# Optimization experiments

Hardware: AMD Instinct MI355X
Metric: run time of the kernel (lower is better)

Reference implementation:

```python
import jax, jax.numpy as jnp
import numpy as np

N, E, C, H = 50000, 250000, 7, 64
D = C + 2  # node feature dim after concatenating labels


def _mlp2(x, w1, b1, w2, b2):
    return jnp.maximum(x @ w1 + b1, 0.0) @ w2 + b2


def _lin(key, fi, fo, bias=True):
    lim = 1.0 / np.sqrt(fi)
    kw, kb = jax.random.split(key)
    w = jax.random.uniform(kw, (fi, fo), jnp.float32, -lim, lim)
    if bias:
        b = jax.random.uniform(kb, (fo,), jnp.float32, -lim, lim)
        return w, b
    return w


def setup_inputs() -> dict:
    key = jax.random.key(0)
    ks = jax.random.split(key, 16)
    v = jax.random.normal(ks[0], (N, C), jnp.float32)
    labels = jnp.zeros((N, 2), jnp.float32).at[0, 1].set(1.0)  # node 0 is the goal
    edge_index = jax.random.randint(ks[1], (2, E), 0, N)
    hx_w1, hx_b1 = _lin(ks[2], 4 * D, H)
    hx_w2, hx_b2 = _lin(ks[3], H, H)
    hy_w1, hy_b1 = _lin(ks[4], 3 * D, H)
    hy_w2, hy_b2 = _lin(ks[5], H, H)
    fx_w1, fx_b1 = _lin(ks[6], 4 * H, H)
    fx_w2, fx_b2 = _lin(ks[7], H, H)
    fy_w1, fy_b1 = _lin(ks[8], 3 * H, H)
    fy_w2, fy_b2 = _lin(ks[9], H, H)
    feta_w1, feta_b1 = _lin(ks[10], H, H)
    feta_w2, feta_b2 = _lin(ks[11], H, H)
    feta_w3 = _lin(ks[12], H, 1, bias=False)
    return dict(v=v, labels=labels, edge_index=edge_index, loop=3,
                hx_w1=hx_w1, hx_b1=hx_b1, hx_w2=hx_w2, hx_b2=hx_b2,
                hy_w1=hy_w1, hy_b1=hy_b1, hy_w2=hy_w2, hy_b2=hy_b2,
                fx_w1=fx_w1, fx_b1=fx_b1, fx_w2=fx_w2, fx_b2=fx_b2,
                fy_w1=fy_w1, fy_b1=fy_b1, fy_w2=fy_w2, fy_b2=fy_b2,
                feta_w1=feta_w1, feta_b1=feta_b1, feta_w2=feta_w2, feta_b2=feta_b2,
                feta_w3=feta_w3)


def reference(v, labels, edge_index, loop,
              hx_w1, hx_b1, hx_w2, hx_b2,
              hy_w1, hy_b1, hy_w2, hy_b2,
              fx_w1, fx_b1, fx_w2, fx_b2,
              fy_w1, fy_b1, fy_w2, fy_b2,
              feta_w1, feta_b1, feta_w2, feta_b2, feta_w3):
    n = v.shape[0]
    vc = jnp.concatenate([v, labels], axis=-1)              # [N, D]
    goal = vc[jnp.argmax(labels[:, 1])][None, :]             # [1, D]
    d = vc - goal
    x = _mlp2(jnp.concatenate([vc, jnp.broadcast_to(goal, vc.shape), d, d * d], -1),
              hx_w1, hx_b1, hx_w2, hx_b2)                    # [N, H]
    src, dst = edge_index[0], edge_index[1]
    vi, vj = vc[src], vc[dst]
    y = _mlp2(jnp.concatenate([vj - vi, vj, vi], -1), hy_w1, hy_b1, hy_w2, hy_b2)  # [E, H]
    for _ in range(loop):
        # MPNN (PyG default flow): x_j = source = edge_index[0], x_i = target = edge_index[1]
        xj_m, xi_m = x[src], x[dst]
        m = _mlp2(jnp.concatenate([xj_m - xi_m, xj_m, xi_m, y], -1),
                  fx_w1, fx_b1, fx_w2, fx_b2)                # [E, H]
        agg = jax.ops.segment_max(m, dst, num_segments=n)    # scatter-max to targets; empty -> -inf
        x = jnp.maximum(x, agg)                              # -inf absorbed by max with x
        xi, xj = x[src], x[dst]                              # Explorer: i=edge_index[0], j=edge_index[1]
        y = jnp.maximum(y, _mlp2(jnp.concatenate([xj - xi, xj, xi], -1),
                                 fy_w1, fy_b1, fy_w2, fy_b2))
    h = jnp.maximum(x @ feta_w1 + feta_b1, 0.0)
    h = jnp.maximum(h @ feta_w2 + feta_b2, 0.0)
    return h @ feta_w3                                       # [N, 1]
```

## Files before the change

### kernel.cpp

```cpp
#include <hip/hip_runtime.h>
#include <math.h>

typedef unsigned short u16;
typedef unsigned int u32;
typedef unsigned long long u64;
typedef __attribute__((ext_vector_type(8))) _Float16 f16x8;
typedef __attribute__((ext_vector_type(2))) _Float16 f16x2;
typedef __attribute__((ext_vector_type(4))) float f32x4;

union U8h { f16x8 v; f16x2 p[4]; u32 u[4]; _Float16 s[8]; };
union U4h { _Float16 s[4]; u64 u; };

__device__ __forceinline__ void atomicMaxF(float* addr, float val) {
  if (val >= 0.0f) {
    atomicMax((int*)addr, __float_as_int(val));
  } else {
    atomicMin((unsigned int*)addr, (unsigned int)__float_as_int(val));
  }
}

__device__ __forceinline__ f16x2 pk(float a, float b) {
  return __builtin_bit_cast(f16x2, __builtin_amdgcn_cvt_pkrtz(a, b));
}

__device__ __forceinline__ void dec8h(const float* f, U8h& h, U8h& l) {
#pragma unroll
// ... 113 lines not shown
  if (c < 64) {
    float s = hxb1[c];
#pragma unroll
    for (int k = 0; k < 9; ++k) s += g[k] * hxw1[(9 + k) * 64 + c];
    b1p[c] = s;
  }
}

__global__ __launch_bounds__(256) void k_prep(const float* __restrict__ fxw1, const float* __restrict__ fxw2,
                                              const float* __restrict__ fyw1, const float* __restrict__ fyw2,
                                              const float* __restrict__ hyw1, const float* __restrict__ hyw2,
                                              const float* __restrict__ hxw1, const float* __restrict__ hxw2,
                                              const float* __restrict__ few1, const float* __restrict__ few2,
                                              _Float16* __restrict__ wp, u64* __restrict__ goalkey) {
  if (blockIdx.x == 0 && threadIdx.x == 0) *goalkey = 0;
  _Float16* fxB1 = wp;
  _Float16* fxB2 = wp + 12288;
  _Float16* fyB1 = wp + 16384;
  _Float16* fyB2 = wp + 24576;
  _Float16* hyB1 = wp + 28672;
  _Float16* hyB2 = wp + 30720;
  _Float16* hxB1 = wp + 34816;
  _Float16* hxB2 = wp + 36864;
  _Float16* feB1 = wp + 40960;
  _Float16* feB2 = wp + 45056;
  int tid = blockIdx.x * 256 + threadIdx.x;
  int which, id;
  _Float16* oh;
  if (tid < 1536)      { which = 0; id = tid;        oh = fxB1; }
  else if (tid < 2048) { which = 1; id = tid - 1536; oh = fxB2; }
  else if (tid < 3072) { which = 2; id = tid - 2048; oh = fyB1; }
  else if (tid < 3584) { which = 3; id = tid - 3072; oh = fyB2; }
  else if (tid < 3840) { which = 4; id = tid - 3584; oh = hyB1; }
  else if (tid < 4352) { which = 5; id = tid - 3840; oh = hyB2; }
  else if (tid < 4608) { which = 6; id = tid - 4352; oh = hxB1; }
  else if (tid < 5120) { which = 7; id = tid - 4608; oh = hxB2; }
  else if (tid < 5632) { which = 8; id = tid - 5120; oh = feB1; }
  else if (tid < 6144) { which = 9; id = tid - 5632; oh = feB2; }
  else return;
  int lane = id & 63;
  int q = lane >> 4, col = lane & 15;
  int c = id >> 8, t = (id >> 6) & 3;
#pragma unroll
  for (int j = 0; j < 8; ++j) {
    int k = c * 32 + q * 8 + j;
    int n = t * 16 + col;
    float w;
    if (which == 0) {
      w = (k < 64)  ? fxw1[k * 64 + n] + fxw1[(k + 64) * 64 + n]
        : (k < 128) ? fxw1[(k + 64) * 64 + n] - fxw1[(k - 64) * 64 + n]
                    : fxw1[(k + 64) * 64 + n];
    } else if (which == 1) {
      w = fxw2[k * 64 + n];
// ... 2 lines not shown
                   : fyw1[(k + 64) * 64 + n] - fyw1[(k - 64) * 64 + n];
    } else if (which == 3) {
      w = fyw2[k * 64 + n];
    } else if (which == 4) {
      if (k <= 8)                  w = hyw1[k * 64 + n] + hyw1[(k + 9) * 64 + n];
      else if (k >= 16 && k <= 24) w = hyw1[(k + 2) * 64 + n] - hyw1[(k - 16) * 64 + n];
      else                         w = 0.f;
    } else if (which == 5) {
      w = hyw2[k * 64 + n];
    } else if (which == 6) {
      w = (k < 9) ? hxw1[k * 64 + n] : (k < 27) ? hxw1[(k + 9) * 64 + n] : 0.f;
    } else if (which == 7) {
      w = hxw2[k * 64 + n];
    } else if (which == 8) {
      w = few1[k * 64 + n];
    } else {
      w = few2[k * 64 + n];
    }
    oh[id * 8 + j] = (_Float16)w;
  }
}

__global__ __launch_bounds__(256) void k_scan1(const int* __restrict__ deg, int N,
                                               int* __restrict__ bsum) {
  __shared__ int red[256];
  int b = blockIdx.x;
  int s = 0;
  for (int i = threadIdx.x; i < 1024; i += 256) {
    int idx = b * 1024 + i;
    s += (idx < N) ? deg[idx] : 0;
  }
  red[threadIdx.x] = s; __syncthreads();
// ... 42 lines not shown
                                                 int* __restrict__ cursor,
                                                 int* __restrict__ srcp, int* __restrict__ dstp) {
  int e = blockIdx.x * 256 + threadIdx.x;
  if (e < E) {
    int d = dst[e];
    int pos = atomicAdd(&cursor[d], 1);
    srcp[pos] = src[e];
    dstp[pos] = d;
  }
}

__global__ __launch_bounds__(256) void k_hx2(
    const float* __restrict__ vcp, const float* __restrict__ goal,
    const _Float16* __restrict__ B1, const float* __restrict__ b1p,
    const _Float16* __restrict__ B2, const float* __restrict__ b2,
    float* __restrict__ xout, float* __restrict__ xout2, _Float16* __restrict__ xh, int N) {
  __shared__ float hbuf[4][16 * 68];
  const int lane = threadIdx.x & 63;
  const int wv = threadIdx.x >> 6;
  const int m = lane & 15, q = lane >> 4;
  const int base = blockIdx.x * 64 + wv * 16;
  int node = base + m; if (node >= N) node = N - 1;
  float vc[12];
  *(float4*)(vc + 0) = *(const float4*)(vcp + (size_t)node * 16);
  *(float4*)(vc + 4) = *(const float4*)(vcp + (size_t)node * 16 + 4);
  *(float4*)(vc + 8) = *(const float4*)(vcp + (size_t)node * 16 + 8);
  float gl[9];
#pragma unroll
  for (int i = 0; i < 9; ++i) gl[i] = goal[i];
  float f[8];
#pragma unroll
// ... 53 lines not shown
  int row = base + m;
  if (row < N) {
    float ov[16];
    const float* orow = hb + m * 68 + q * 16;
    *(float4*)(ov + 0)  = *(const float4*)(orow);
    *(float4*)(ov + 4)  = *(const float4*)(orow + 4);
    *(float4*)(ov + 8)  = *(const float4*)(orow + 8);
    *(float4*)(ov + 12) = *(const float4*)(orow + 12);
    float* p1 = xout + (size_t)row * 64 + q * 16;
    float* p2 = xout2 + (size_t)row * 64 + q * 16;
#pragma unroll
    for (int i = 0; i < 4; ++i) {
      *(float4*)(p1 + i * 4) = *(const float4*)(ov + i * 4);
      *(float4*)(p2 + i * 4) = *(const float4*)(ov + i * 4);
    }
    U8h X0, X1;
    conv8_rne(ov + 0, X0);
    conv8_rne(ov + 8, X1);
    *(f16x8*)(xh + (size_t)row * 64 + q * 16)     = X0.v;
    *(f16x8*)(xh + (size_t)row * 64 + q * 16 + 8) = X1.v;
  }
}

__global__ __launch_bounds__(256) void k_cc(const float4* __restrict__ s,
                                            float4* __restrict__ d,
                                            _Float16* __restrict__ h16, int n4) {
  int i = blockIdx.x * 256 + threadIdx.x;
  if (i < n4) {
    float4 v = s[i];
    d[i] = v;
    U4h o;
    o.s[0] = (_Float16)v.x; o.s[1] = (_Float16)v.y;
    o.s[2] = (_Float16)v.z; o.s[3] = (_Float16)v.w;
    *(u64*)(h16 + (size_t)i * 4) = o.u;
  }
}

__global__ __launch_bounds__(256) void k_hyfx(
    const float* __restrict__ vcp, const _Float16* __restrict__ xh,
    const int* __restrict__ src, const int* __restrict__ dst,
    const _Float16* __restrict__ hB1, const float* __restrict__ hb1,
    const _Float16* __restrict__ hB2, const float* __restrict__ hb2,
    const _Float16* __restrict__ xB1, const float* __restrict__ xb1,
    const _Float16* __restrict__ xB2, const float* __restrict__ xb2,
    _Float16* __restrict__ y, float* __restrict__ xnew, int E) {
  __shared__ float hbuf[4][16 * 68];
  const int lane = threadIdx.x & 63;
  const int wv = threadIdx.x >> 6;
  const int m = lane & 15, q = lane >> 4;
  const int base = blockIdx.x * 64 + wv * 16;
  int em = base + m; if (em >= E) em = E - 1;
  const int si = src[em], di = dst[em];
  const int row = base + m;
  const bool live = row < E;

  const int node = (q < 2) ? di : si;
  const float* p = vcp + (size_t)node * 16 + (q & 1) * 8;
  float f[8];
  *(float4*)(f + 0) = *(const float4*)(p);
  *(float4*)(f + 4) = *(const float4*)(p + 4);
  const _Float16* ps = xh + (size_t)si * 64 + q * 8;
  const _Float16* pd = xh + (size_t)di * 64 + q * 8;
  U8h Xs0, Xs1, Xd0, Xd1;
  Xs0.v = *(const f16x8*)ps;         Xs1.v = *(const f16x8*)(ps + 32);
  Xd0.v = *(const f16x8*)pd;         Xd1.v = *(const f16x8*)(pd + 32);

  U8h Ah, Al;
  dec8h(f, Ah, Al);

  f32x4 acc[4];
#pragma unroll
  for (int t = 0; t < 4; ++t) { float bv = hb1[t * 16 + m]; acc[t] = (f32x4){bv, bv, bv, bv}; }
#pragma unroll
  for (int t = 0; t < 4; ++t) {
    f16x8 b = *(const f16x8*)(hB1 + ((size_t)t * 64 + lane) * 8);
    acc[t] = __builtin_amdgcn_mfma_f32_16x16x32_f16(Ah.v, b, acc[t], 0, 0, 0);
    acc[t] = __builtin_amdgcn_mfma_f32_16x16x32_f16(Al.v, b, acc[t], 0, 0, 0);
  }

  float* hb = hbuf[wv];
#pragma unroll
  for (int t = 0; t < 4; ++t)
#pragma unroll
    for (int r = 0; r < 4; ++r)
      hb[(q * 4 + r) * 68 + t * 16 + m] = fmaxf(acc[t][r], 0.f);

  float fh[16];
  load_row(hb + m * 68 + q * 8, fh);
  U8h H0, H1;
  conv8_rne(fh + 0, H0);
  conv8_rne(fh + 8, H1);

  f32x4 o[4];
#pragma unroll
  for (int t = 0; t < 4; ++t) { float bv = hb2[t * 16 + m]; o[t] = (f32x4){bv, bv, bv, bv}; }
#pragma unroll
  for (int t = 0; t < 4; ++t) {
    f16x8 b0 = *(const f16x8*)(hB2 + ((size_t)(0 * 4 + t) * 64 + lane) * 8);
    f16x8 b1_ = *(const f16x8*)(hB2 + ((size_t)(1 * 4 + t) * 64 + lane) * 8);
    o[t] = __builtin_amdgcn_mfma_f32_16x16x32_f16(H0.v, b0, o[t], 0, 0, 0);
    o[t] = __builtin_amdgcn_mfma_f32_16x16x32_f16(H1.v, b1_, o[t], 0, 0, 0);
  }

#pragma unroll
  for (int t = 0; t < 4; ++t)
#pragma unroll
    for (int r = 0; r < 4; ++r)
      hb[(q * 4 + r) * 68 + t * 16 + m] = o[t][r];

  float nv[16];
  load_row(hb + m * 68 + q * 8, nv);
  U8h Yh0, Yh1;
  conv8_rne(nv + 0, Yh0);
  conv8_rne(nv + 8, Yh1);
  if (live) {
    size_t yo = (size_t)row * 64 + q * 8;
    *(f16x8*)(y + yo)      = Yh0.v;
    *(f16x8*)(y + yo + 32) = Yh1.v;
  }

  f32x4 acc2[4];
#pragma unroll
  for (int t = 0; t < 4; ++t) { float bv = xb1[t * 16 + m]; acc2[t] = (f32x4){bv, bv, bv, bv}; }
#pragma unroll
  for (int t = 0; t < 4; ++t) {
    f16x8 b0 = *(const f16x8*)(xB1 + ((size_t)(0 * 4 + t) * 64 + lane) * 8);
    f16x8 b1_ = *(const f16x8*)(xB1 + ((size_t)(1 * 4 + t) * 64 + lane) * 8);
    f16x8 b2_ = *(const f16x8*)(xB1 + ((size_t)(2 * 4 + t) * 64 + lane) * 8);
    f16x8 b3_ = *(const f16x8*)(xB1 + ((size_t)(3 * 4 + t) * 64 + lane) * 8);
    f16x8 b4_ = *(const f16x8*)(xB1 + ((size_t)(4 * 4 + t) * 64 + lane) * 8);
    f16x8 b5_ = *(const f16x8*)(xB1 + ((size_t)(5 * 4 + t) * 64 + lane) * 8);
    acc2[t] = __builtin_amdgcn_mfma_f32_16x16x32_f16(Xs0.v, b0, acc2[t], 0, 0, 0);
    acc2[t] = __builtin_amdgcn_mfma_f32_16x16x32_f16(Xs1.v, b1_, acc2[t], 0, 0, 0);
    acc2[t] = __builtin_amdgcn_mfma_f32_16x16x32_f16(Xd0.v, b2_, acc2[t], 0, 0, 0);
    acc2[t] = __builtin_amdgcn_mfma_f32_16x16x32_f16(Xd1.v, b3_, acc2[t], 0, 0, 0);
    acc2[t] = __builtin_amdgcn_mfma_f32_16x16x32_f16(Yh0.v, b4_, acc2[t], 0, 0, 0);
    acc2[t] = __builtin_amdgcn_mfma_f32_16x16x32_f16(Yh1.v, b5_, acc2[t], 0, 0, 0);
  }

#pragma unroll
  for (int t = 0; t < 4; ++t)
#pragma unroll
    for (int r = 0; r < 4; ++r)
      hb[(q * 4 + r) * 68 + t * 16 + m] = fmaxf(acc2[t][r], 0.f);

  float fh2[16];
  load_row(hb + m * 68 + q * 8, fh2);
  U8h G0, G1;
  conv8_rne(fh2 + 0, G0);
  conv8_rne(fh2 + 8, G1);

  f32x4 o2[4];
#pragma unroll
  for (int t = 0; t < 4; ++t) { float bv = xb2[t * 16 + m]; o2[t] = (f32x4){bv, bv, bv, bv}; }
#pragma unroll
  for (int t = 0; t < 4; ++t) {
    f16x8 b0 = *(const f16x8*)(xB2 + ((size_t)(0 * 4 + t) * 64 + lane) * 8);
    f16x8 b1_ = *(const f16x8*)(xB2 + ((size_t)(1 * 4 + t) * 64 + lane) * 8);
    o2[t] = __builtin_amdgcn_mfma_f32_16x16x32_f16(G0.v, b0, o2[t], 0, 0, 0);
    o2[t] = __builtin_amdgcn_mfma_f32_16x16x32_f16(G1.v, b1_, o2[t], 0, 0, 0);
  }

  int dd[4];
  int e0 = base + q * 4;
#pragma unroll
  for (int r = 0; r < 4; ++r) {
    int e2 = e0 + r;
    dd[r] = (e2 < E) ? dst[e2] : -1;
  }
  RunCtx rc = run_ctx(dd, lane, q);
#pragma unroll
  for (int t = 0; t < 4; ++t) emit_t(o2[t], dd, rc, lane, m, t, xnew);
}

__global__ __launch_bounds__(256) void k_fyfx(
    const _Float16* __restrict__ xh, _Float16* __restrict__ y,
    const int* __restrict__ src, const int* __restrict__ dst,
    const _Float16* __restrict__ yB1, const float* __restrict__ yb1,
    const _Float16* __restrict__ yB2, const float* __restrict__ yb2,
    const _Float16* __restrict__ xB1, const float* __restrict__ xb1,
    const _Float16* __restrict__ xB2, const float* __restrict__ xb2,
    float* __restrict__ xnew, int E, int storeY) {
  __shared__ float hbuf[4][16 * 68];
  const int lane = threadIdx.x & 63;
  const int wv = threadIdx.x >> 6;
  const int m = lane & 15, q = lane >> 4;
  const int base = blockIdx.x * 64 + wv * 16;
  int em = base + m; if (em >= E) em = E - 1;
  const int si = src[em], di = dst[em];
  const int row = base + m;
  const bool live = row < E;

  const _Float16* ps = xh + (size_t)si * 64 + q * 8;
  const _Float16* pd = xh + (size_t)di * 64 + q * 8;
  U8h Xs0, Xs1, Xd0, Xd1;
  Xs0.v = *(const f16x8*)ps;         Xs1.v = *(const f16x8*)(ps + 32);
  Xd0.v = *(const f16x8*)pd;         Xd1.v = *(const f16x8*)(pd + 32);
  U8h Ho0, Ho1;
  {
    size_t yo = (size_t)em * 64 + q * 8;
    Ho0.v = *(const f16x8*)(y + yo);  Ho1.v = *(const f16x8*)(y + yo + 32);
  }

  f32x4 acc[4];
#pragma unroll
  for (int t = 0; t < 4; ++t) { float bv = yb1[t * 16 + m]; acc[t] = (f32x4){bv, bv, bv, bv}; }
#pragma unroll
  for (int t = 0; t < 4; ++t) {
    f16x8 b0 = *(const f16x8*)(yB1 + ((size_t)(0 * 4 + t) * 64 + lane) * 8);
    f16x8 b1_ = *(const f16x8*)(yB1 + ((size_t)(1 * 4 + t) * 64 + lane) * 8);
    f16x8 b2_ = *(const f16x8*)(yB1 + ((size_t)(2 * 4 + t) * 64 + lane) * 8);
    f16x8 b3_ = *(const f16x8*)(yB1 + ((size_t)(3 * 4 + t) * 64 + lane) * 8);
    acc[t] = __builtin_amdgcn_mfma_f32_16x16x32_f16(Xd0.v, b0, acc[t], 0, 0, 0);
    acc[t] = __builtin_amdgcn_mfma_f32_16x16x32_f16(Xd1.v, b1_, acc[t], 0, 0, 0);
    acc[t] = __builtin_amdgcn_mfma_f32_16x16x32_f16(Xs0.v, b2_, acc[t], 0, 0, 0);
    acc[t] = __builtin_amdgcn_mfma_f32_16x16x32_f16(Xs1.v, b3_, acc[t], 0, 0, 0);
  }

  float* hb = hbuf[wv];
#pragma unroll
  for (int t = 0; t < 4; ++t)
#pragma unroll
    for (int r = 0; r < 4; ++r)
      hb[(q * 4 + r) * 68 + t * 16 + m] = fmaxf(acc[t][r], 0.f);

  float fh[16];
  load_row(hb + m * 68 + q * 8, fh);
  U8h H0, H1;
  conv8_rne(fh + 0, H0);
  conv8_rne(fh + 8, H1);

  f32x4 o[4];
#pragma unroll
  for (int t = 0; t < 4; ++t) { float bv = yb2[t * 16 + m]; o[t] = (f32x4){bv, bv, bv, bv}; }
#pragma unroll
  for (int t = 0; t < 4; ++t) {
    f16x8 b0 = *(const f16x8*)(yB2 + ((size_t)(0 * 4 + t) * 64 + lane) * 8);
    f16x8 b1_ = *(const f16x8*)(yB2 + ((size_t)(1 * 4 + t) * 64 + lane) * 8);
    o[t] = __builtin_amdgcn_mfma_f32_16x16x32_f16(H0.v, b0, o[t], 0, 0, 0);
    o[t] = __builtin_amdgcn_mfma_f32_16x16x32_f16(H1.v, b1_, o[t], 0, 0, 0);
  }

#pragma unroll
  for (int t = 0; t < 4; ++t)
#pragma unroll
    for (int r = 0; r < 4; ++r)
      hb[(q * 4 + r) * 68 + t * 16 + m] = o[t][r];

  float nv[16];
  load_row(hb + m * 68 + q * 8, nv);
#pragma unroll
  for (int i = 0; i < 8; ++i) {
    nv[i]     = fmaxf((float)Ho0.s[i], nv[i]);
    nv[8 + i] = fmaxf((float)Ho1.s[i], nv[8 + i]);
  }
  U8h Yh0, Yh1;
  conv8_rne(nv + 0, Yh0);
  conv8_rne(nv + 8, Yh1);
  if (live && storeY) {
    size_t yo = (size_t)row * 64 + q * 8;
    *(f16x8*)(y + yo)      = Yh0.v;
    *(f16x8*)(y + yo + 32) = Yh1.v;
  }

  f32x4 acc2[4];
#pragma unroll
  for (int t = 0; t < 4; ++t) { float bv = xb1[t * 16 + m]; acc2[t] = (f32x4){bv, bv, bv, bv}; }
#pragma unroll
  for (int t = 0; t < 4; ++t) {
    f16x8 b0 = *(const f16x8*)(xB1 + ((size_t)(0 * 4 + t) * 64 + lane) * 8);
    f16x8 b1_ = *(const f16x8*)(xB1 + ((size_t)(1 * 4 + t) * 64 + lane) * 8);
    f16x8 b2_ = *(const f16x8*)(xB1 + ((size_t)(2 * 4 + t) * 64 + lane) * 8);
    f16x8 b3_ = *(const f16x8*)(xB1 + ((size_t)(3 * 4 + t) * 64 + lane) * 8);
    f16x8 b4_ = *(const f16x8*)(xB1 + ((size_t)(4 * 4 + t) * 64 + lane) * 8);
    f16x8 b5_ = *(const f16x8*)(xB1 + ((size_t)(5 * 4 + t) * 64 + lane) * 8);
    acc2[t] = __builtin_amdgcn_mfma_f32_16x16x32_f16(Xs0.v, b0, acc2[t], 0, 0, 0);
    acc2[t] = __builtin_amdgcn_mfma_f32_16x16x32_f16(Xs1.v, b1_, acc2[t], 0, 0, 0);
    acc2[t] = __builtin_amdgcn_mfma_f32_16x16x32_f16(Xd0.v, b2_, acc2[t], 0, 0, 0);
    acc2[t] = __builtin_amdgcn_mfma_f32_16x16x32_f16(Xd1.v, b3_, acc2[t], 0, 0, 0);
    acc2[t] = __builtin_amdgcn_mfma_f32_16x16x32_f16(Yh0.v, b4_, acc2[t], 0, 0, 0);
    acc2[t] = __builtin_amdgcn_mfma_f32_16x16x32_f16(Yh1.v, b5_, acc2[t], 0, 0, 0);
  }

#pragma unroll
  for (int t = 0; t < 4; ++t)
#pragma unroll
    for (int r = 0; r < 4; ++r)
      hb[(q * 4 + r) * 68 + t * 16 + m] = fmaxf(acc2[t][r], 0.f);

  float fh2[16];
  load_row(hb + m * 68 + q * 8, fh2);
  U8h G0, G1;
  conv8_rne(fh2 + 0, G0);
  conv8_rne(fh2 + 8, G1);

  f32x4 o2[4];
#pragma unroll
  for (int t = 0; t < 4; ++t) { float bv = xb2[t * 16 + m]; o2[t] = (f32x4){bv, bv, bv, bv}; }
#pragma unroll
  for (int t = 0; t < 4; ++t) {
    f16x8 b0 = *(const f16x8*)(xB2 + ((size_t)(0 * 4 + t) * 64 + lane) * 8);
    f16x8 b1_ = *(const f16x8*)(xB2 + ((size_t)(1 * 4 + t) * 64 + lane) * 8);
    o2[t] = __builtin_amdgcn_mfma_f32_16x16x32_f16(G0.v, b0, o2[t], 0, 0, 0);
    o2[t] = __builtin_amdgcn_mfma_f32_16x16x32_f16(G1.v, b1_, o2[t], 0, 0, 0);
  }

  int dd[4];
  int e0 = base + q * 4;
#pragma unroll
  for (int r = 0; r < 4; ++r) {
    int e2 = e0 + r;
    dd[r] = (e2 < E) ? dst[e2] : -1;
  }
  RunCtx rc = run_ctx(dd, lane, q);
#pragma unroll
  for (int t = 0; t < 4; ++t) emit_t(o2[t], dd, rc, lane, m, t, xnew);
}

__global__ __launch_bounds__(256) void k_feta2(
// ... 96 lines not shown
  const float* feta_w2 = (const float*)d_in[22];
  const float* feta_b2 = (const float*)d_in[23];
  const float* feta_w3 = (const float*)d_in[24];

  int N = in_sizes[0] / 7;
  int E = in_sizes[2] / 2;
  const int* src = ei;
  const int* dst = ei + E;

  char* wsb = (char*)d_ws;
  float* goal = (float*)wsb;
  u64* goalkey = (u64*)(wsb + 64);
  float* b1p = (float*)(wsb + 96);
  float* xa = (float*)(wsb + 512);
  float* xb = xa + (size_t)N * 64;
  _Float16* xh = (_Float16*)(xb + (size_t)N * 64);
  _Float16* y = xh + (size_t)N * 64;
  _Float16* wp = y + (size_t)E * 64;
  float* vcp = (float*)(wp + 49152);
  int* deg = (int*)(vcp + (size_t)N * 16);
  int* cursor = deg + N;
  int* srcp = cursor + N;
  int* dstp = srcp + E;
  int* bsum = dstp + E;

  _Float16* fxB1 = wp;          _Float16* fxB2 = wp + 12288;
  _Float16* fyB1 = wp + 16384;  _Float16* fyB2 = wp + 24576;
  _Float16* hyB1 = wp + 28672;  _Float16* hyB2 = wp + 30720;
  _Float16* hxB1 = wp + 34816;  _Float16* hxB2 = wp + 36864;
  _Float16* feB1 = wp + 40960;  _Float16* feB2 = wp + 45056;

  int SB = (N + 1023) / 1024;

  hipMemsetAsync(deg, 0, (size_t)N * 4, stream);
  k_prep<<<24, 256, 0, stream>>>(fx_w1, fx_w2, fy_w1, fy_w2, hy_w1, hy_w2,
                                 hx_w1, hx_w2, feta_w1, feta_w2, wp, goalkey);
  k_vch<<<(N * 16 + 255) / 256, 256, 0, stream>>>(v, labels, vcp, N, dst, E, deg, goalkey);
  k_goal2b<<<1, 64, 0, stream>>>(v, labels, goalkey, hx_w1, hx_b1, goal, b1p);
  k_scan1<<<SB, 256, 0, stream>>>(deg, N, bsum);
  k_scan3<<<SB, 256, 0, stream>>>(deg, bsum, N, cursor);
  k_scatter<<<(E + 255) / 256, 256, 0, stream>>>(src, dst, E, cursor, srcp, dstp);

  k_hx2<<<(N + 63) / 64, 256, 0, stream>>>(vcp, goal, hxB1, b1p, hxB2, hx_b2, xa, xb, xh, N);

  int EB = (E + 63) / 64;
  k_hyfx<<<EB, 256, 0, stream>>>(vcp, xh, srcp, dstp,
                                 hyB1, hy_b1, hyB2, hy_b2,
                                 fxB1, fx_b1, fxB2, fx_b2, y, xb, E);
  k_cc<<<(N * 16 + 255) / 256, 256, 0, stream>>>((const float4*)xb, (float4*)xa, xh, N * 16);
  k_fyfx<<<EB, 256, 0, stream>>>(xh, y, srcp, dstp,
                                 fyB1, fy_b1, fyB2, fy_b2,
                                 fxB1, fx_b1, fxB2, fx_b2, xa, E, 1);
  k_cc<<<(N * 16 + 255) / 256, 256, 0, stream>>>((const float4*)xa, (float4*)xb, xh, N * 16);
  k_fyfx<<<EB, 256, 0, stream>>>(xh, y, srcp, dstp,
                                 fyB1, fy_b1, fyB2, fy_b2,
                                 fxB1, fx_b1, fxB2, fx_b2, xb, E, 0);

  k_feta2<<<(N + 63) / 64, 256, 0, stream>>>(xb, feB1, feta_b1, feB2, feta_b2, feta_w3,
                                             (float*)d_out, N);
}
```

Measured before the change: 342.4 us.

## Precompute per-node first-layer projections and gather them in edge kernels

The first-layer matmuls of the edge MLPs are linear in the source and destination node features, so they are split into per-node projections. A new node kernel computes these with MFMA and stores four 64-wide fp16 slots per node (256 halves). The edge kernel then gathers and adds the projected slots instead of running the K=128 or K=384 MFMAs per edge, keeping only the y-part of the fx first layer and the second layers. This trades per-edge MFMA work for extra node-level passes and a larger per-node gather (512 bytes per node instead of 128). It also rounds the projections to fp16 before the bias add and ReLU.

```diff
diff --git a/kernel.cpp b/kernel.cpp
--- a/kernel.cpp
+++ b/kernel.cpp
@@ -9,7 +9,6 @@
 typedef __attribute__((ext_vector_type(4))) float f32x4;
 
 union U8h { f16x8 v; f16x2 p[4]; u32 u[4]; _Float16 s[8]; };
-union U4h { _Float16 s[4]; u64 u; };
 
 __device__ __forceinline__ void atomicMaxF(float* addr, float val) {
   if (val >= 0.0f) {
@@ -153,29 +152,31 @@
                                               const float* __restrict__ few1, const float* __restrict__ few2,
                                               _Float16* __restrict__ wp, u64* __restrict__ goalkey) {
   if (blockIdx.x == 0 && threadIdx.x == 0) *goalkey = 0;
-  _Float16* fxB1 = wp;
-  _Float16* fxB2 = wp + 12288;
-  _Float16* fyB1 = wp + 16384;
-  _Float16* fyB2 = wp + 24576;
-  _Float16* hyB1 = wp + 28672;
-  _Float16* hyB2 = wp + 30720;
-  _Float16* hxB1 = wp + 34816;
-  _Float16* hxB2 = wp + 36864;
-  _Float16* feB1 = wp + 40960;
-  _Float16* feB2 = wp + 45056;
+  _Float16* fxB1  = wp;
+  _Float16* fxB2  = wp + 12288;
+  _Float16* fyB1  = wp + 16384;
+  _Float16* fyB2  = wp + 24576;
+  _Float16* hyB1  = wp + 28672;
+  _Float16* hyB2  = wp + 30720;
+  _Float16* hxB1  = wp + 34816;
+  _Float16* hxB2  = wp + 36864;
+  _Float16* feB1  = wp + 40960;
+  _Float16* feB2  = wp + 45056;
+  _Float16* hyB1s = wp + 49152;
   int tid = blockIdx.x * 256 + threadIdx.x;
   int which, id;
   _Float16* oh;
-  if (tid < 1536)      { which = 0; id = tid;        oh = fxB1; }
-  else if (tid < 2048) { which = 1; id = tid - 1536; oh = fxB2; }
-  else if (tid < 3072) { which = 2; id = tid - 2048; oh = fyB1; }
-  else if (tid < 3584) { which = 3; id = tid - 3072; oh = fyB2; }
-  else if (tid < 3840) { which = 4; id = tid - 3584; oh = hyB1; }
-  else if (tid < 4352) { which = 5; id = tid - 3840; oh = hyB2; }
-  else if (tid < 4608) { which = 6; id = tid - 4352; oh = hxB1; }
-  else if (tid < 5120) { which = 7; id = tid - 4608; oh = hxB2; }
-  else if (tid < 5632) { which = 8; id = tid - 5120; oh = feB1; }
-  else if (tid < 6144) { which = 9; id = tid - 5632; oh = feB2; }
+  if (tid < 1536)      { which = 0;  id = tid;        oh = fxB1; }
+  else if (tid < 2048) { which = 1;  id = tid - 1536; oh = fxB2; }
+  else if (tid < 3072) { which = 2;  id = tid - 2048; oh = fyB1; }
+  else if (tid < 3584) { which = 3;  id = tid - 3072; oh = fyB2; }
+  else if (tid < 3840) { which = 4;  id = tid - 3584; oh = hyB1; }
+  else if (tid < 4352) { which = 5;  id = tid - 3840; oh = hyB2; }
+  else if (tid < 4608) { which = 6;  id = tid - 4352; oh = hxB1; }
+  else if (tid < 5120) { which = 7;  id = tid - 4608; oh = hxB2; }
+  else if (tid < 5632) { which = 8;  id = tid - 5120; oh = feB1; }
+  else if (tid < 6144) { which = 9;  id = tid - 5632; oh = feB2; }
+  else if (tid < 6400) { which = 10; id = tid - 6144; oh = hyB1s; }
   else return;
   int lane = id & 63;
   int q = lane >> 4, col = lane & 15;
@@ -208,8 +209,10 @@
       w = hxw2[k * 64 + n];
     } else if (which == 8) {
       w = few1[k * 64 + n];
+    } else if (which == 9) {
+      w = few2[k * 64 + n];
     } else {
-      w = few2[k * 64 + n];
+      w = (k < 9) ? hyw1[(k + 18) * 64 + n] - hyw1[k * 64 + n] : 0.f;
     }
     oh[id * 8 + j] = (_Float16)w;
   }
@@ -282,7 +285,7 @@
     const float* __restrict__ vcp, const float* __restrict__ goal,
     const _Float16* __restrict__ B1, const float* __restrict__ b1p,
     const _Float16* __restrict__ B2, const float* __restrict__ b2,
-    float* __restrict__ xout, float* __restrict__ xout2, _Float16* __restrict__ xh, int N) {
+    float* __restrict__ xout, float* __restrict__ xout2, int N) {
   __shared__ float hbuf[4][16 * 68];
   const int lane = threadIdx.x & 63;
   const int wv = threadIdx.x >> 6;
@@ -366,245 +369,210 @@
       *(float4*)(p1 + i * 4) = *(const float4*)(ov + i * 4);
       *(float4*)(p2 + i * 4) = *(const float4*)(ov + i * 4);
     }
-    U8h X0, X1;
-    conv8_rne(ov + 0, X0);
-    conv8_rne(ov + 8, X1);
-    *(f16x8*)(xh + (size_t)row * 64 + q * 16)     = X0.v;
-    *(f16x8*)(xh + (size_t)row * 64 + q * 16 + 8) = X1.v;
-  }
-}
-
-__global__ __launch_bounds__(256) void k_cc(const float4* __restrict__ s,
-                                            float4* __restrict__ d,
-                                            _Float16* __restrict__ h16, int n4) {
-  int i = blockIdx.x * 256 + threadIdx.x;
-  if (i < n4) {
-    float4 v = s[i];
-    d[i] = v;
-    U4h o;
-    o.s[0] = (_Float16)v.x; o.s[1] = (_Float16)v.y;
-    o.s[2] = (_Float16)v.z; o.s[3] = (_Float16)v.w;
-    *(u64*)(h16 + (size_t)i * 4) = o.u;
-  }
-}
-
-__global__ __launch_bounds__(256) void k_hyfx(
-    const float* __restrict__ vcp, const _Float16* __restrict__ xh,
+  }
+}
+
+__global__ __launch_bounds__(256) void k_proj(
+    const float* __restrict__ x,
+    const _Float16* __restrict__ fyB1, const _Float16* __restrict__ fxB1,
+    _Float16* __restrict__ P, float* __restrict__ xcopy, int N) {
+  __shared__ float hbuf[4][16 * 68];
+  const int lane = threadIdx.x & 63;
+  const int wv = threadIdx.x >> 6;
+  const int m = lane & 15, q = lane >> 4;
+  const int base = blockIdx.x * 64 + wv * 16;
+  int node = base + m; if (node >= N) node = N - 1;
+  const int row = base + m;
+  const bool live = row < N;
+
+  float xr[16];
+  load_row(x + (size_t)node * 64 + q * 8, xr);
+  U8h X0, X1;
+  conv8_rne(xr + 0, X0);
+  conv8_rne(xr + 8, X1);
+  if (live) {
+    float* pc = xcopy + (size_t)row * 64;
+    *(float4*)(pc + q * 8)      = *(const float4*)(xr + 0);
+    *(float4*)(pc + q * 8 + 4)  = *(const float4*)(xr + 4);
+    *(float4*)(pc + 32 + q * 8)     = *(const float4*)(xr + 8);
+    *(float4*)(pc + 32 + q * 8 + 4) = *(const float4*)(xr + 12);
+  }
+
+  float* hb = hbuf[wv];
+#pragma unroll
+  for (int p = 0; p < 4; ++p) {
+    const _Float16* W = (p == 0 || p == 2) ? fyB1 : fxB1;
+    const int c0 = (p == 0 || p == 3) ? 2 : 0;
+    const int slot = p * 64;
+    f32x4 o[4];
+#pragma unroll
+    for (int t = 0; t < 4; ++t) o[t] = (f32x4){0.f, 0.f, 0.f, 0.f};
+#pragma unroll
+    for (int t = 0; t < 4; ++t) {
+      f16x8 b0 = *(const f16x8*)(W + ((size_t)((c0 + 0) * 4 + t) * 64 + lane) * 8);
+      f16x8 b1 = *(const f16x8*)(W + ((size_t)((c0 + 1) * 4 + t) * 64 + lane) * 8);
+      o[t] = __builtin_amdgcn_mfma_f32_16x16x32_f16(X0.v, b0, o[t], 0, 0, 0);
+      o[t] = __builtin_amdgcn_mfma_f32_16x16x32_f16(X1.v, b1, o[t], 0, 0, 0);
+    }
+#pragma unroll
+    for (int t = 0; t < 4; ++t)
+#pragma unroll
+      for (int r = 0; r < 4; ++r)
+        hb[(q * 4 + r) * 68 + t * 16 + m] = o[t][r];
+    float pv[16];
+    load_row(hb + m * 68 + q * 8, pv);
+    U8h P0, P1;
+    conv8_rne(pv + 0, P0);
+    conv8_rne(pv + 8, P1);
+    if (live) {
+      _Float16* pp = P + (size_t)row * 256 + slot;
+      *(f16x8*)(pp + q * 8)      = P0.v;
+      *(f16x8*)(pp + 32 + q * 8) = P1.v;
+    }
+  }
+}
+
+__global__ __launch_bounds__(256) void k_proj0(
+    const float* __restrict__ vcp, const float* __restrict__ x,
+    const _Float16* __restrict__ hyB1, const _Float16* __restrict__ hyB1s,
+    const _Float16* __restrict__ fxB1,
+    _Float16* __restrict__ P, int N) {
+  __shared__ float hbuf[4][16 * 68];
+  const int lane = threadIdx.x & 63;
+  const int wv = threadIdx.x >> 6;
+  const int m = lane & 15, q = lane >> 4;
+  const int base = blockIdx.x * 64 + wv * 16;
+  int node = base + m; if (node >= N) node = N - 1;
+  const int row = base + m;
+  const bool live = row < N;
+
+  float vr[8] = {0.f, 0.f, 0.f, 0.f, 0.f, 0.f, 0.f, 0.f};
+  if (q < 2) {
+    *(float4*)(vr + 0) = *(const float4*)(vcp + (size_t)node * 16 + q * 8);
+    *(float4*)(vr + 4) = *(const float4*)(vcp + (size_t)node * 16 + q * 8 + 4);
+  }
+  U8h V0;
+  conv8_rne(vr, V0);
+  float xr[16];
+  load_row(x + (size_t)node * 64 + q * 8, xr);
+  U8h X0, X1;
+  conv8_rne(xr + 0, X0);
+  conv8_rne(xr + 8, X1);
+
+  float* hb = hbuf[wv];
+#pragma unroll
+  for (int p = 0; p < 4; ++p) {
+    const int slot = p * 64;
+    f32x4 o[4];
+#pragma unroll
+    for (int t = 0; t < 4; ++t) o[t] = (f32x4){0.f, 0.f, 0.f, 0.f};
+    if (p == 0 || p == 2) {
+      const _Float16* W = (p == 0) ? hyB1s : hyB1;
+#pragma unroll
+      for (int t = 0; t < 4; ++t) {
+        f16x8 b = *(const f16x8*)(W + ((size_t)t * 64 + lane) * 8);
+        o[t] = __builtin_amdgcn_mfma_f32_16x16x32_f16(V0.v, b, o[t], 0, 0, 0);
+      }
+    } else {
+      const int c0 = (p == 1) ? 0 : 2;
+#pragma unroll
+      for (int t = 0; t < 4; ++t) {
+        f16x8 b0 = *(const f16x8*)(fxB1 + ((size_t)((c0 + 0) * 4 + t) * 64 + lane) * 8);
+        f16x8 b1 = *(const f16x8*)(fxB1 + ((size_t)((c0 + 1) * 4 + t) * 64 + lane) * 8);
+        o[t] = __builtin_amdgcn_mfma_f32_16x16x32_f16(X0.v, b0, o[t], 0, 0, 0);
+        o[t] = __builtin_amdgcn_mfma_f32_16x16x32_f16(X1.v, b1, o[t], 0, 0, 0);
+      }
+    }
+#pragma unroll
+    for (int t = 0; t < 4; ++t)
+#pragma unroll
+      for (int r = 0; r < 4; ++r)
+        hb[(q * 4 + r) * 68 + t * 16 + m] = o[t][r];
+    float pv[16];
+    load_row(hb + m * 68 + q * 8, pv);
+    U8h P0, P1;
+    conv8_rne(pv + 0, P0);
+    conv8_rne(pv + 8, P1);
+    if (live) {
+      _Float16* pp = P + (size_t)row * 256 + slot;
+      *(f16x8*)(pp + q * 8)      = P0.v;
+      *(f16x8*)(pp + 32 + q * 8) = P1.v;
+    }
+  }
+}
+
+__global__ __launch_bounds__(256) void k_edge(
+    const _Float16* __restrict__ P, _Float16* __restrict__ y,
     const int* __restrict__ src, const int* __restrict__ dst,
-    const _Float16* __restrict__ hB1, const float* __restrict__ hb1,
-    const _Float16* __restrict__ hB2, const float* __restrict__ hb2,
+    const float* __restrict__ yb1,
+    const _Float16* __restrict__ yB2, const float* __restrict__ yb2,
     const _Float16* __restrict__ xB1, const float* __restrict__ xb1,
     const _Float16* __restrict__ xB2, const float* __restrict__ xb2,
-    _Float16* __restrict__ y, float* __restrict__ xnew, int E) {
+    float* __restrict__ xnew, int E, int useOldY, int storeY) {
   __shared__ float hbuf[4][16 * 68];
   const int lane = threadIdx.x & 63;
   const int wv = threadIdx.x >> 6;
   const int m = lane & 15, q = lane >> 4;
   const int base = blockIdx.x * 64 + wv * 16;
   int em = base + m; if (em >= E) em = E - 1;
-  const int si = src[em], di = dst[em];
+  const int s = src[em], d = dst[em];
   const int row = base + m;
   const bool live = row < E;
 
-  const int node = (q < 2) ? di : si;
-  const float* p = vcp + (size_t)node * 16 + (q & 1) * 8;
-  float f[8];
-  *(float4*)(f + 0) = *(const float4*)(p);
-  *(float4*)(f + 4) = *(const float4*)(p + 4);
-  const _Float16* ps = xh + (size_t)si * 64 + q * 8;
-  const _Float16* pd = xh + (size_t)di * 64 + q * 8;
-  U8h Xs0, Xs1, Xd0, Xd1;
-  Xs0.v = *(const f16x8*)ps;         Xs1.v = *(const f16x8*)(ps + 32);
-  Xd0.v = *(const f16x8*)pd;         Xd1.v = *(const f16x8*)(pd + 32);
-
-  U8h Ah, Al;
-  dec8h(f, Ah, Al);
-
-  f32x4 acc[4];
-#pragma unroll
-  for (int t = 0; t < 4; ++t) { float bv = hb1[t * 16 + m]; acc[t] = (f32x4){bv, bv, bv, bv}; }
+  const _Float16* Ps = P + (size_t)s * 256;
+  const _Float16* Pd = P + (size_t)d * 256 + 128;
+  U8h Bf0, Bf1, Cf0, Cf1, Af0, Af1, Df0, Df1;
+  Bf0.v = *(const f16x8*)(Ps + q * 8);       Bf1.v = *(const f16x8*)(Ps + 32 + q * 8);
+  Cf0.v = *(const f16x8*)(Ps + 64 + q * 8);  Cf1.v = *(const f16x8*)(Ps + 96 + q * 8);
+  Af0.v = *(const f16x8*)(Pd + q * 8);       Af1.v = *(const f16x8*)(Pd + 32 + q * 8);
+  Df0.v = *(const f16x8*)(Pd + 64 + q * 8);  Df1.v = *(const f16x8*)(Pd + 96 + q * 8);
+  U8h Ho0, Ho1;
+  if (useOldY) {
+    size_t yo = (size_t)em * 64 + q * 8;
+    Ho0.v = *(const f16x8*)(y + yo);
+    Ho1.v = *(const f16x8*)(y + yo + 32);
+  }
+
+  float bias1[16];
+  *(float4*)(bias1 + 0)  = *(const float4*)(yb1 + q * 8);
+  *(float4*)(bias1 + 4)  = *(const float4*)(yb1 + q * 8 + 4);
+  *(float4*)(bias1 + 8)  = *(const float4*)(yb1 + 32 + q * 8);
+  *(float4*)(bias1 + 12) = *(const float4*)(yb1 + 32 + q * 8 + 4);
+  float hrow[16];
+#pragma unroll
+  for (int i = 0; i < 8; ++i) {
+    hrow[i]     = fmaxf((float)Af0.s[i] + (float)Bf0.s[i] + bias1[i], 0.f);
+    hrow[8 + i] = fmaxf((float)Af1.s[i] + (float)Bf1.s[i] + bias1[8 + i], 0.f);
+  }
+  U8h H0, H1;
+  conv8_rne(hrow + 0, H0);
+  conv8_rne(hrow + 8, H1);
+
+  f32x4 o[4];
+#pragma unroll
+  for (int t = 0; t < 4; ++t) { float bv = yb2[t * 16 + m]; o[t] = (f32x4){bv, bv, bv, bv}; }
 #pragma unroll
   for (int t = 0; t < 4; ++t) {
-    f16x8 b = *(const f16x8*)(hB1 + ((size_t)t * 64 + lane) * 8);
-    acc[t] = __builtin_amdgcn_mfma_f32_16x16x32_f16(Ah.v, b, acc[t], 0, 0, 0);
-    acc[t] = __builtin_amdgcn_mfma_f32_16x16x32_f16(Al.v, b, acc[t], 0, 0, 0);
+    f16x8 b0 = *(const f16x8*)(yB2 + ((size_t)(0 * 4 + t) * 64 + lane) * 8);
+    f16x8 b1 = *(const f16x8*)(yB2 + ((size_t)(1 * 4 + t) * 64 + lane) * 8);
+    o[t] = __builtin_amdgcn_mfma_f32_16x16x32_f16(H0.v, b0, o[t], 0, 0, 0);
+    o[t] = __builtin_amdgcn_mfma_f32_16x16x32_f16(H1.v, b1, o[t], 0, 0, 0);
   }
 
   float* hb = hbuf[wv];
-#pragma unroll
-  for (int t = 0; t < 4; ++t)
-#pragma unroll
-    for (int r = 0; r < 4; ++r)
-      hb[(q * 4 + r) * 68 + t * 16 + m] = fmaxf(acc[t][r], 0.f);
-
-  float fh[16];
-  load_row(hb + m * 68 + q * 8, fh);
-  U8h H0, H1;
-  conv8_rne(fh + 0, H0);
-  conv8_rne(fh + 8, H1);
-
-  f32x4 o[4];
-#pragma unroll
-  for (int t = 0; t < 4; ++t) { float bv = hb2[t * 16 + m]; o[t] = (f32x4){bv, bv, bv, bv}; }
-#pragma unroll
-  for (int t = 0; t < 4; ++t) {
-    f16x8 b0 = *(const f16x8*)(hB2 + ((size_t)(0 * 4 + t) * 64 + lane) * 8);
-    f16x8 b1_ = *(const f16x8*)(hB2 + ((size_t)(1 * 4 + t) * 64 + lane) * 8);
-    o[t] = __builtin_amdgcn_mfma_f32_16x16x32_f16(H0.v, b0, o[t], 0, 0, 0);
-    o[t] = __builtin_amdgcn_mfma_f32_16x16x32_f16(H1.v, b1_, o[t], 0, 0, 0);
-  }
-
 #pragma unroll
   for (int t = 0; t < 4; ++t)
 #pragma unroll
     for (int r = 0; r < 4; ++r)
       hb[(q * 4 + r) * 68 + t * 16 + m] = o[t][r];
-
   float nv[16];
   load_row(hb + m * 68 + q * 8, nv);
-  U8h Yh0, Yh1;
-  conv8_rne(nv + 0, Yh0);
-  conv8_rne(nv + 8, Yh1);
-  if (live) {
-    size_t yo = (size_t)row * 64 + q * 8;
-    *(f16x8*)(y + yo)      = Yh0.v;
-    *(f16x8*)(y + yo + 32) = Yh1.v;
-  }
-
-  f32x4 acc2[4];
-#pragma unroll
-  for (int t = 0; t < 4; ++t) { float bv = xb1[t * 16 + m]; acc2[t] = (f32x4){bv, bv, bv, bv}; }
-#pragma unroll
-  for (int t = 0; t < 4; ++t) {
-    f16x8 b0 = *(const f16x8*)(xB1 + ((size_t)(0 * 4 + t) * 64 + lane) * 8);
-    f16x8 b1_ = *(const f16x8*)(xB1 + ((size_t)(1 * 4 + t) * 64 + lane) * 8);
-    f16x8 b2_ = *(const f16x8*)(xB1 + ((size_t)(2 * 4 + t) * 64 + lane) * 8);
-    f16x8 b3_ = *(const f16x8*)(xB1 + ((size_t)(3 * 4 + t) * 64 + lane) * 8);
-    f16x8 b4_ = *(const f16x8*)(xB1 + ((size_t)(4 * 4 + t) * 64 + lane) * 8);
-    f16x8 b5_ = *(const f16x8*)(xB1 + ((size_t)(5 * 4 + t) * 64 + lane) * 8);
-    acc2[t] = __builtin_amdgcn_mfma_f32_16x16x32_f16(Xs0.v, b0, acc2[t], 0, 0, 0);
-    acc2[t] = __builtin_amdgcn_mfma_f32_16x16x32_f16(Xs1.v, b1_, acc2[t], 0, 0, 0);
-    acc2[t] = __builtin_amdgcn_mfma_f32_16x16x32_f16(Xd0.v, b2_, acc2[t], 0, 0, 0);
-    acc2[t] = __builtin_amdgcn_mfma_f32_16x16x32_f16(Xd1.v, b3_, acc2[t], 0, 0, 0);
-    acc2[t] = __builtin_amdgcn_mfma_f32_16x16x32_f16(Yh0.v, b4_, acc2[t], 0, 0, 0);
-    acc2[t] = __builtin_amdgcn_mfma_f32_16x16x32_f16(Yh1.v, b5_, acc2[t], 0, 0, 0);
-  }
-
-#pragma unroll
-  for (int t = 0; t < 4; ++t)
-#pragma unroll
-    for (int r = 0; r < 4; ++r)
-      hb[(q * 4 + r) * 68 + t * 16 + m] = fmaxf(acc2[t][r], 0.f);
-
-  float fh2[16];
-  load_row(hb + m * 68 + q * 8, fh2);
-  U8h G0, G1;
-  conv8_rne(fh2 + 0, G0);
-  conv8_rne(fh2 + 8, G1);
-
-  f32x4 o2[4];
-#pragma unroll
-  for (int t = 0; t < 4; ++t) { float bv = xb2[t * 16 + m]; o2[t] = (f32x4){bv, bv, bv, bv}; }
-#pragma unroll
-  for (int t = 0; t < 4; ++t) {
-    f16x8 b0 = *(const f16x8*)(xB2 + ((size_t)(0 * 4 + t) * 64 + lane) * 8);
-    f16x8 b1_ = *(const f16x8*)(xB2 + ((size_t)(1 * 4 + t) * 64 + lane) * 8);
-    o2[t] = __builtin_amdgcn_mfma_f32_16x16x32_f16(G0.v, b0, o2[t], 0, 0, 0);
-    o2[t] = __builtin_amdgcn_mfma_f32_16x16x32_f16(G1.v, b1_, o2[t], 0, 0, 0);
-  }
-
-  int dd[4];
-  int e0 = base + q * 4;
-#pragma unroll
-  for (int r = 0; r < 4; ++r) {
-    int e2 = e0 + r;
-    dd[r] = (e2 < E) ? dst[e2] : -1;
-  }
-  RunCtx rc = run_ctx(dd, lane, q);
-#pragma unroll
-  for (int t = 0; t < 4; ++t) emit_t(o2[t], dd, rc, lane, m, t, xnew);
-}
-
-__global__ __launch_bounds__(256) void k_fyfx(
-    const _Float16* __restrict__ xh, _Float16* __restrict__ y,
-    const int* __restrict__ src, const int* __restrict__ dst,
-    const _Float16* __restrict__ yB1, const float* __restrict__ yb1,
-    const _Float16* __restrict__ yB2, const float* __restrict__ yb2,
-    const _Float16* __restrict__ xB1, const float* __restrict__ xb1,
-    const _Float16* __restrict__ xB2, const float* __restrict__ xb2,
-    float* __restrict__ xnew, int E, int storeY) {
-  __shared__ float hbuf[4][16 * 68];
-  const int lane = threadIdx.x & 63;
-  const int wv = threadIdx.x >> 6;
-  const int m = lane & 15, q = lane >> 4;
-  const int base = blockIdx.x * 64 + wv * 16;
-  int em = base + m; if (em >= E) em = E - 1;
-  const int si = src[em], di = dst[em];
-  const int row = base + m;
-  const bool live = row < E;
-
-  const _Float16* ps = xh + (size_t)si * 64 + q * 8;
-  const _Float16* pd = xh + (size_t)di * 64 + q * 8;
-  U8h Xs0, Xs1, Xd0, Xd1;
-  Xs0.v = *(const f16x8*)ps;         Xs1.v = *(const f16x8*)(ps + 32);
-  Xd0.v = *(const f16x8*)pd;         Xd1.v = *(const f16x8*)(pd + 32);
-  U8h Ho0, Ho1;
-  {
-    size_t yo = (size_t)em * 64 + q * 8;
-    Ho0.v = *(const f16x8*)(y + yo);  Ho1.v = *(const f16x8*)(y + yo + 32);
-  }
-
-  f32x4 acc[4];
-#pragma unroll
-  for (int t = 0; t < 4; ++t) { float bv = yb1[t * 16 + m]; acc[t] = (f32x4){bv, bv, bv, bv}; }
-#pragma unroll
-  for (int t = 0; t < 4; ++t) {
-    f16x8 b0 = *(const f16x8*)(yB1 + ((size_t)(0 * 4 + t) * 64 + lane) * 8);
-    f16x8 b1_ = *(const f16x8*)(yB1 + ((size_t)(1 * 4 + t) * 64 + lane) * 8);
-    f16x8 b2_ = *(const f16x8*)(yB1 + ((size_t)(2 * 4 + t) * 64 + lane) * 8);
-    f16x8 b3_ = *(const f16x8*)(yB1 + ((size_t)(3 * 4 + t) * 64 + lane) * 8);
-    acc[t] = __builtin_amdgcn_mfma_f32_16x16x32_f16(Xd0.v, b0, acc[t], 0, 0, 0);
-    acc[t] = __builtin_amdgcn_mfma_f32_16x16x32_f16(Xd1.v, b1_, acc[t], 0, 0, 0);
-    acc[t] = __builtin_amdgcn_mfma_f32_16x16x32_f16(Xs0.v, b2_, acc[t], 0, 0, 0);
-    acc[t] = __builtin_amdgcn_mfma_f32_16x16x32_f16(Xs1.v, b3_, acc[t], 0, 0, 0);
-  }
-
-  float* hb = hbuf[wv];
-#pragma unroll
-  for (int t = 0; t < 4; ++t)
-#pragma unroll
-    for (int r = 0; r < 4; ++r)
-      hb[(q * 4 + r) * 68 + t * 16 + m] = fmaxf(acc[t][r], 0.f);
-
-  float fh[16];
-  load_row(hb + m * 68 + q * 8, fh);
-  U8h H0, H1;
-  conv8_rne(fh + 0, H0);
-  conv8_rne(fh + 8, H1);
-
-  f32x4 o[4];
-#pragma unroll
-  for (int t = 0; t < 4; ++t) { float bv = yb2[t * 16 + m]; o[t] = (f32x4){bv, bv, bv, bv}; }
-#pragma unroll
-  for (int t = 0; t < 4; ++t) {
-    f16x8 b0 = *(const f16x8*)(yB2 + ((size_t)(0 * 4 + t) * 64 + lane) * 8);
-    f16x8 b1_ = *(const f16x8*)(yB2 + ((size_t)(1 * 4 + t) * 64 + lane) * 8);
-    o[t] = __builtin_amdgcn_mfma_f32_16x16x32_f16(H0.v, b0, o[t], 0, 0, 0);
-    o[t] = __builtin_amdgcn_mfma_f32_16x16x32_f16(H1.v, b1_, o[t], 0, 0, 0);
-  }
-
-#pragma unroll
-  for (int t = 0; t < 4; ++t)
-#pragma unroll
-    for (int r = 0; r < 4; ++r)
-      hb[(q * 4 + r) * 68 + t * 16 + m] = o[t][r];
-
-  float nv[16];
-  load_row(hb + m * 68 + q * 8, nv);
-#pragma unroll
-  for (int i = 0; i < 8; ++i) {
-    nv[i]     = fmaxf((float)Ho0.s[i], nv[i]);
-    nv[8 + i] = fmaxf((float)Ho1.s[i], nv[8 + i]);
+  if (useOldY) {
+#pragma unroll
+    for (int i = 0; i < 8; ++i) {
+      nv[i]     = fmaxf(nv[i], (float)Ho0.s[i]);
+      nv[8 + i] = fmaxf(nv[8 + i], (float)Ho1.s[i]);
+    }
   }
   U8h Yh0, Yh1;
   conv8_rne(nv + 0, Yh0);
@@ -615,36 +583,33 @@
     *(f16x8*)(y + yo + 32) = Yh1.v;
   }
 
-  f32x4 acc2[4];
-#pragma unroll
-  for (int t = 0; t < 4; ++t) { float bv = xb1[t * 16 + m]; acc2[t] = (f32x4){bv, bv, bv, bv}; }
+  f32x4 a2[4];
+#pragma unroll
+  for (int t = 0; t < 4; ++t) { float bv = xb1[t * 16 + m]; a2[t] = (f32x4){bv, bv, bv, bv}; }
 #pragma unroll
   for (int t = 0; t < 4; ++t) {
-    f16x8 b0 = *(const f16x8*)(xB1 + ((size_t)(0 * 4 + t) * 64 + lane) * 8);
-    f16x8 b1_ = *(const f16x8*)(xB1 + ((size_t)(1 * 4 + t) * 64 + lane) * 8);
-    f16x8 b2_ = *(const f16x8*)(xB1 + ((size_t)(2 * 4 + t) * 64 + lane) * 8);
-    f16x8 b3_ = *(const f16x8*)(xB1 + ((size_t)(3 * 4 + t) * 64 + lane) * 8);
-    f16x8 b4_ = *(const f16x8*)(xB1 + ((size_t)(4 * 4 + t) * 64 + lane) * 8);
-    f16x8 b5_ = *(const f16x8*)(xB1 + ((size_t)(5 * 4 + t) * 64 + lane) * 8);
-    acc2[t] = __builtin_amdgcn_mfma_f32_16x16x32_f16(Xs0.v, b0, acc2[t], 0, 0, 0);
-    acc2[t] = __builtin_amdgcn_mfma_f32_16x16x32_f16(Xs1.v, b1_, acc2[t], 0, 0, 0);
-    acc2[t] = __builtin_amdgcn_mfma_f32_16x16x32_f16(Xd0.v, b2_, acc2[t], 0, 0, 0);
-    acc2[t] = __builtin_amdgcn_mfma_f32_16x16x32_f16(Xd1.v, b3_, acc2[t], 0, 0, 0);
-    acc2[t] = __builtin_amdgcn_mfma_f32_16x16x32_f16(Yh0.v, b4_, acc2[t], 0, 0, 0);
-    acc2[t] = __builtin_amdgcn_mfma_f32_16x16x32_f16(Yh1.v, b5_, acc2[t], 0, 0, 0);
-  }
-
+    f16x8 b4 = *(const f16x8*)(xB1 + ((size_t)(4 * 4 + t) * 64 + lane) * 8);
+    f16x8 b5 = *(const f16x8*)(xB1 + ((size_t)(5 * 4 + t) * 64 + lane) * 8);
+    a2[t] = __builtin_amdgcn_mfma_f32_16x16x32_f16(Yh0.v, b4, a2[t], 0, 0, 0);
+    a2[t] = __builtin_amdgcn_mfma_f32_16x16x32_f16(Yh1.v, b5, a2[t], 0, 0, 0);
+  }
 #pragma unroll
   for (int t = 0; t < 4; ++t)
 #pragma unroll
     for (int r = 0; r < 4; ++r)
-      hb[(q * 4 + r) * 68 + t * 16 + m] = fmaxf(acc2[t][r], 0.f);
-
-  float fh2[16];
-  load_row(hb + m * 68 + q * 8, fh2);
+      hb[(q * 4 + r) * 68 + t * 16 + m] = a2[t][r];
+  float pyv[16];
+  load_row(hb + m * 68 + q * 8, pyv);
+
+  float g[16];
+#pragma unroll
+  for (int i = 0; i < 8; ++i) {
+    g[i]     = fmaxf((float)Cf0.s[i] + (float)Df0.s[i] + pyv[i], 0.f);
+    g[8 + i] = fmaxf((float)Cf1.s[i] + (float)Df1.s[i] + pyv[8 + i], 0.f);
+  }
   U8h G0, G1;
-  conv8_rne(fh2 + 0, G0);
-  conv8_rne(fh2 + 8, G1);
+  conv8_rne(g + 0, G0);
+  conv8_rne(g + 8, G1);
 
   f32x4 o2[4];
 #pragma unroll
@@ -652,9 +617,9 @@
 #pragma unroll
   for (int t = 0; t < 4; ++t) {
     f16x8 b0 = *(const f16x8*)(xB2 + ((size_t)(0 * 4 + t) * 64 + lane) * 8);
-    f16x8 b1_ = *(const f16x8*)(xB2 + ((size_t)(1 * 4 + t) * 64 + lane) * 8);
+    f16x8 b1 = *(const f16x8*)(xB2 + ((size_t)(1 * 4 + t) * 64 + lane) * 8);
     o2[t] = __builtin_amdgcn_mfma_f32_16x16x32_f16(G0.v, b0, o2[t], 0, 0, 0);
-    o2[t] = __builtin_amdgcn_mfma_f32_16x16x32_f16(G1.v, b1_, o2[t], 0, 0, 0);
+    o2[t] = __builtin_amdgcn_mfma_f32_16x16x32_f16(G1.v, b1, o2[t], 0, 0, 0);
   }
 
   int dd[4];
@@ -781,26 +746,27 @@
   float* b1p = (float*)(wsb + 96);
   float* xa = (float*)(wsb + 512);
   float* xb = xa + (size_t)N * 64;
-  _Float16* xh = (_Float16*)(xb + (size_t)N * 64);
-  _Float16* y = xh + (size_t)N * 64;
-  _Float16* wp = y + (size_t)E * 64;
-  float* vcp = (float*)(wp + 49152);
+  _Float16* y = (_Float16*)(xb + (size_t)N * 64);
+  _Float16* P = y + (size_t)E * 64;
+  _Float16* wp = P + (size_t)N * 256;
+  float* vcp = (float*)(wp + 51200);
   int* deg = (int*)(vcp + (size_t)N * 16);
   int* cursor = deg + N;
   int* srcp = cursor + N;
   int* dstp = srcp + E;
   int* bsum = dstp + E;
 
-  _Float16* fxB1 = wp;          _Float16* fxB2 = wp + 12288;
-  _Float16* fyB1 = wp + 16384;  _Float16* fyB2 = wp + 24576;
-  _Float16* hyB1 = wp + 28672;  _Float16* hyB2 = wp + 30720;
-  _Float16* hxB1 = wp + 34816;  _Float16* hxB2 = wp + 36864;
-  _Float16* feB1 = wp + 40960;  _Float16* feB2 = wp + 45056;
+  _Float16* fxB1  = wp;          _Float16* fxB2 = wp + 12288;
+  _Float16* fyB1  = wp + 16384;  _Float16* fyB2 = wp + 24576;
+  _Float16* hyB1  = wp + 28672;  _Float16* hyB2 = wp + 30720;
+  _Float16* hxB1  = wp + 34816;  _Float16* hxB2 = wp + 36864;
+  _Float16* feB1  = wp + 40960;  _Float16* feB2 = wp + 45056;
+  _Float16* hyB1s = wp + 49152;
 
   int SB = (N + 1023) / 1024;
 
   hipMemsetAsync(deg, 0, (size_t)N * 4, stream);
-  k_prep<<<24, 256, 0, stream>>>(fx_w1, fx_w2, fy_w1, fy_w2, hy_w1, hy_w2,
+  k_prep<<<25, 256, 0, stream>>>(fx_w1, fx_w2, fy_w1, fy_w2, hy_w1, hy_w2,
                                  hx_w1, hx_w2, feta_w1, feta_w2, wp, goalkey);
   k_vch<<<(N * 16 + 255) / 256, 256, 0, stream>>>(v, labels, vcp, N, dst, E, deg, goalkey);
   k_goal2b<<<1, 64, 0, stream>>>(v, labels, goalkey, hx_w1, hx_b1, goal, b1p);
@@ -808,21 +774,20 @@
   k_scan3<<<SB, 256, 0, stream>>>(deg, bsum, N, cursor);
   k_scatter<<<(E + 255) / 256, 256, 0, stream>>>(src, dst, E, cursor, srcp, dstp);
 
-  k_hx2<<<(N + 63) / 64, 256, 0, stream>>>(vcp, goal, hxB1, b1p, hxB2, hx_b2, xa, xb, xh, N);
-
+  int NB = (N + 63) / 64;
   int EB = (E + 63) / 64;
-  k_hyfx<<<EB, 256, 0, stream>>>(vcp, xh, srcp, dstp,
-                                 hyB1, hy_b1, hyB2, hy_b2,
-                                 fxB1, fx_b1, fxB2, fx_b2, y, xb, E);
-  k_cc<<<(N * 16 + 255) / 256, 256, 0, stream>>>((const float4*)xb, (float4*)xa, xh, N * 16);
-  k_fyfx<<<EB, 256, 0, stream>>>(xh, y, srcp, dstp,
-                                 fyB1, fy_b1, fyB2, fy_b2,
-                                 fxB1, fx_b1, fxB2, fx_b2, xa, E, 1);
-  k_cc<<<(N * 16 + 255) / 256, 256, 0, stream>>>((const float4*)xa, (float4*)xb, xh, N * 16);
-  k_fyfx<<<EB, 256, 0, stream>>>(xh, y, srcp, dstp,
-                                 fyB1, fy_b1, fyB2, fy_b2,
-                                 fxB1, fx_b1, fxB2, fx_b2, xb, E, 0);
-
-  k_feta2<<<(N + 63) / 64, 256, 0, stream>>>(xb, feB1, feta_b1, feB2, feta_b2, feta_w3,
-                                             (float*)d_out, N);
-}
+
+  k_hx2<<<NB, 256, 0, stream>>>(vcp, goal, hxB1, b1p, hxB2, hx_b2, xa, xb, N);
+  k_proj0<<<NB, 256, 0, stream>>>(vcp, xa, hyB1, hyB1s, fxB1, P, N);
+  k_edge<<<EB, 256, 0, stream>>>(P, y, srcp, dstp, hy_b1, hyB2, hy_b2,
+                                 fxB1, fx_b1, fxB2, fx_b2, xb, E, 0, 1);
+  k_proj<<<NB, 256, 0, stream>>>(xb, fyB1, fxB1, P, xa, N);
+  k_edge<<<EB, 256, 0, stream>>>(P, y, srcp, dstp, fy_b1, fyB2, fy_b2,
+                                 fxB1, fx_b1, fxB2, fx_b2, xa, E, 1, 1);
+  k_proj<<<NB, 256, 0, stream>>>(xa, fyB1, fxB1, P, xb, N);
+  k_edge<<<EB, 256, 0, stream>>>(P, y, srcp, dstp, fy_b1, fyB2, fy_b2,
+                                 fxB1, fx_b1, fxB2, fx_b2, xb, E, 1, 0);
+
+  k_feta2<<<NB, 256, 0, stream>>>(xb, feB1, feta_b1, feB2, feta_b2, feta_w3,
+                                  (float*)d_out, N);
+}
```

After: 363.9 us. +6.3%, slower.
